# Optimization experiments

Hardware: AMD Instinct MI355X
Metric: run time of the kernel (lower is better)

The kernel has to match this reference:

```python
import jax, jax.numpy as jnp
import numpy as np

DIM = 512
VOCAB = 32000
G = 0.9


def setup_inputs() -> dict:
    key = jax.random.key(0)
    k1, k2, k3, k4, k5, k6 = jax.random.split(key, 6)
    B, T = 32, 4096
    x = jax.random.randint(k1, (B, T), 0, VOCAB)
    s = 1.0 / np.sqrt(DIM)
    emb = jax.random.normal(k2, (VOCAB, DIM), dtype=jnp.float32)
    W_w = jax.random.uniform(k3, (DIM, DIM), dtype=jnp.float32, minval=-s, maxval=s)
    W_b = jax.random.uniform(k4, (DIM,), dtype=jnp.float32, minval=-s, maxval=s)
    head_w = jax.random.uniform(k5, (VOCAB, DIM), dtype=jnp.float32, minval=-s, maxval=s)
    head_b = jax.random.uniform(k6, (VOCAB,), dtype=jnp.float32, minval=-s, maxval=s)
    return {"x": x, "emb": emb, "W_w": W_w, "W_b": W_b, "head_w": head_w, "head_b": head_b}


def reference(x, emb, W_w, W_b, head_w, head_b):
    # u_t = tanh(W @ emb(x_t) + b): input-only nonlinearity, computed for all t at once
    u = jnp.tanh(jnp.einsum('btd,ed->bte', emb[x], W_w) + W_b)  # [B,T,D]
    B = x.shape[0]
    h0 = jnp.zeros((B, DIM), dtype=u.dtype)

    def step(h, u_t):  # h = g*h + (1-g)*u_t  (leaky integration)
        h = G * h + (1.0 - G) * u_t
        return h, None

    h, _ = jax.lax.scan(step, h0, jnp.swapaxes(u, 0, 1))  # scan over T
    return h @ head_w.T + head_b  # [B, VOCAB]
```

## Files before the change

### kernel.cpp

```cpp
#include <hip/hip_runtime.h>
#include <math.h>
#include <stdint.h>

#define B_  32
#define T_  4096
#define D_  512
#define V_  32000
#define KW  128

typedef __attribute__((ext_vector_type(8))) short bf16x8_t;
typedef __attribute__((ext_vector_type(4))) float f32x4_t;

__device__ inline unsigned short f2bf(float f) {
    union { float f; uint32_t u; } c; c.f = f;
    return (unsigned short)((c.u + 0x7FFFu + ((c.u >> 16) & 1u)) >> 16);
}
__device__ inline float bf2f(unsigned short s) {
    union { uint32_t u; float f; } c; c.u = ((uint32_t)s) << 16;
    return c.f;
}

__global__ __launch_bounds__(256) void k_cvtw(const float* __restrict__ Ww,
                                              unsigned short* __restrict__ Wbf,
                                              float* __restrict__ hbuf) {
    const int gid = blockIdx.x * 256 + threadIdx.x;
    const int idx = gid * 8;
    const float4 a = *(const float4*)&Ww[idx];
    const float4 b = *(const float4*)&Ww[idx + 4];
    union { unsigned short s[8]; uint4 v; } o;
    o.s[0] = f2bf(a.x); o.s[1] = f2bf(a.y); o.s[2] = f2bf(a.z); o.s[3] = f2bf(a.w);
    o.s[4] = f2bf(b.x); o.s[5] = f2bf(b.y); o.s[6] = f2bf(b.z); o.s[7] = f2bf(b.w);
    *(uint4*)&Wbf[idx] = o.v;
    if (gid < B_ * D_) hbuf[gid] = 0.f;
}

__global__ __launch_bounds__(256) void k_hidden(const int* __restrict__ x,
                                                const float* __restrict__ emb,
                                                const unsigned short* __restrict__ Wbf,
                                                const float* __restrict__ Wb,
                                                float* __restrict__ h) {
    __shared__ int rows[32];
    __shared__ __align__(16) unsigned short As[32 * 32];
    __shared__ __align__(16) unsigned short Bs[64 * 32];
    __shared__ float red[8][64];

    const int tid = threadIdx.x;
    const int b   = blockIdx.x >> 5;
    const int e0  = ((blockIdx.x >> 2) & 7) * 64;
    const int tb  = blockIdx.x & 3;

    if (tid < 32) rows[tid] = x[b * T_ + (T_ - KW) + tb * 32 + tid];
    __syncthreads();

    const int lane = tid & 63;
    const int w    = tid >> 6;
    const int m15  = lane & 15;
    const int q    = lane >> 4;
    const int mt   = w & 1;
    const int nh   = w >> 1;

    f32x4_t acc[2];
    acc[0] = (f32x4_t){0.f, 0.f, 0.f, 0.f};
    acc[1] = (f32x4_t){0.f, 0.f, 0.f, 0.f};

    for (int k0 = 0; k0 < D_; k0 += 32) {
        __syncthreads();
        if (tid < 128) {
            const float* src = emb + (size_t)rows[tid >> 2] * D_ + k0 + (tid & 3) * 8;
            const float4 a0 = *(const float4*)src;
            const float4 a1 = *(const float4*)(src + 4);
            union { unsigned short s[8]; uint4 v; } o;
            o.s[0] = f2bf(a0.x); o.s[1] = f2bf(a0.y); o.s[2] = f2bf(a0.z); o.s[3] = f2bf(a0.w);
            o.s[4] = f2bf(a1.x); o.s[5] = f2bf(a1.y); o.s[6] = f2bf(a1.z); o.s[7] = f2bf(a1.w);
            *(uint4*)&As[tid * 8] = o.v;
        }
        {
            const unsigned short* src = Wbf + (size_t)(e0 + (tid >> 2)) * D_ + k0 + (tid & 3) * 8;
            __builtin_amdgcn_global_load_lds(
                (const __attribute__((address_space(1))) void*)src,
                (__attribute__((address_space(3))) void*)&Bs[tid * 8], 16, 0, 0);
        }
        __syncthreads();

        const bf16x8_t af  = *(const bf16x8_t*)&As[(mt * 16 + m15) * 32 + q * 8];
        const bf16x8_t bf0 = *(const bf16x8_t*)&Bs[(nh * 32 + m15) * 32 + q * 8];
        const bf16x8_t bf1 = *(const bf16x8_t*)&Bs[(nh * 32 + 16 + m15) * 32 + q * 8];
        acc[0] = __builtin_amdgcn_mfma_f32_16x16x32_bf16(af, bf0, acc[0], 0, 0, 0);
        acc[1] = __builtin_amdgcn_mfma_f32_16x16x32_bf16(af, bf1, acc[1], 0, 0, 0);
    }

    float p[2] = {0.f, 0.f};
#pragma unroll
    for (int ni = 0; ni < 2; ni++) {
        const float wbv = Wb[e0 + nh * 32 + ni * 16 + m15];
#pragma unroll
        for (int r = 0; r < 4; r++) {
            const int twin = tb * 32 + mt * 16 + q * 4 + r;
            const float pre = acc[ni][r] + wbv;
            const float e2  = __expf(2.f * pre);
            const float u   = (e2 - 1.f) / (e2 + 1.f);
            const float wt  = 0.1f * exp2f((float)(127 - twin) * -0.15200309344504995f);
            p[ni] += wt * u;
        }
    }
#pragma unroll
    for (int ni = 0; ni < 2; ni++)
        red[mt * 4 + q][nh * 32 + ni * 16 + m15] = p[ni];
    __syncthreads();
    if (tid < 64) {
        float s = 0.f;
#pragma unroll
        for (int g = 0; g < 8; g++) s += red[g][tid];
        atomicAdd(&h[b * D_ + e0 + tid], s);
    }
}

__global__ __launch_bounds__(256) void k_hsplit(const float* __restrict__ h,
                                                unsigned short* __restrict__ hhi,
                                                unsigned short* __restrict__ hlo) {
    const int i = blockIdx.x * 256 + threadIdx.x;
    const float v = h[i];
    const unsigned short hi = f2bf(v);
    hhi[i] = hi;
    hlo[i] = f2bf(v - bf2f(hi));
}

__global__ __launch_bounds__(256) void k_head(const unsigned short* __restrict__ hhi,
                                              const unsigned short* __restrict__ hlo,
                                              const float* __restrict__ Whead,
                                              const float* __restrict__ bhead,
                                              float* __restrict__ out) {
    const int lane = threadIdx.x & 63;
    const int w    = threadIdx.x >> 6;
    const int n    = lane & 15;
    const int q    = lane >> 4;
    const int v    = blockIdx.x * 64 + w * 16 + n;

    f32x4_t acc[2];
    acc[0] = (f32x4_t){0.f, 0.f, 0.f, 0.f};
    acc[1] = (f32x4_t){0.f, 0.f, 0.f, 0.f};

    const float* __restrict__ wp = Whead + (size_t)v * D_ + q * 8;
    const unsigned short* __restrict__ ah0 = hhi + n * D_ + q * 8;
    const unsigned short* __restrict__ ah1 = hhi + (16 + n) * D_ + q * 8;
    const unsigned short* __restrict__ al0 = hlo + n * D_ + q * 8;
    const unsigned short* __restrict__ al1 = hlo + (16 + n) * D_ + q * 8;

#pragma unroll 2
    for (int ks = 0; ks < 16; ks++) {
        const int off = ks * 32;
        const float4 w0 = *(const float4*)&wp[off];
        const float4 w1 = *(const float4*)&wp[off + 4];
        const bf16x8_t a0h = *(const bf16x8_t*)&ah0[off];
        const bf16x8_t a1h = *(const bf16x8_t*)&ah1[off];
        const bf16x8_t a0l = *(const bf16x8_t*)&al0[off];
        const bf16x8_t a1l = *(const bf16x8_t*)&al1[off];

        const float wf[8] = {w0.x, w0.y, w0.z, w0.w, w1.x, w1.y, w1.z, w1.w};
        union { unsigned short s[8]; bf16x8_t v; } bh, bl;
#pragma unroll
        for (int j = 0; j < 8; j++) {
            const unsigned short hi = f2bf(wf[j]);
            bh.s[j] = hi;
            bl.s[j] = f2bf(wf[j] - bf2f(hi));
        }
        acc[0] = __builtin_amdgcn_mfma_f32_16x16x32_bf16(a0h, bh.v, acc[0], 0, 0, 0);
        acc[1] = __builtin_amdgcn_mfma_f32_16x16x32_bf16(a1h, bh.v, acc[1], 0, 0, 0);
        acc[0] = __builtin_amdgcn_mfma_f32_16x16x32_bf16(a0l, bh.v, acc[0], 0, 0, 0);
        acc[1] = __builtin_amdgcn_mfma_f32_16x16x32_bf16(a1l, bh.v, acc[1], 0, 0, 0);
        acc[0] = __builtin_amdgcn_mfma_f32_16x16x32_bf16(a0h, bl.v, acc[0], 0, 0, 0);
        acc[1] = __builtin_amdgcn_mfma_f32_16x16x32_bf16(a1h, bl.v, acc[1], 0, 0, 0);
    }

    const float bb = bhead[v];
#pragma unroll
    for (int mtl = 0; mtl < 2; mtl++)
#pragma unroll
        for (int r = 0; r < 4; r++)
            out[(size_t)(mtl * 16 + q * 4 + r) * V_ + v] = acc[mtl][r] + bb;
}

extern "C" void kernel_launch(void* const* d_in, const int* in_sizes, int n_in,
                              void* d_out, int out_size, void* d_ws, size_t ws_size,
                              hipStream_t stream) {
    const int*   x      = (const int*)d_in[0];
    const float* emb    = (const float*)d_in[1];
    const float* W_w    = (const float*)d_in[2];
    const float* W_b    = (const float*)d_in[3];
    const float* head_w = (const float*)d_in[4];
    const float* head_b = (const float*)d_in[5];
    float* out = (float*)d_out;

    unsigned short* Wbf = (unsigned short*)d_ws;
    float*          hbuf = (float*)((char*)d_ws + 512 * 1024);
    unsigned short* hhi  = (unsigned short*)((char*)d_ws + 576 * 1024);
    unsigned short* hlo  = (unsigned short*)((char*)d_ws + 608 * 1024);

    k_cvtw  <<<dim3(128),     dim3(256), 0, stream>>>(W_w, Wbf, hbuf);
    k_hidden<<<dim3(1024),    dim3(256), 0, stream>>>(x, emb, Wbf, W_b, hbuf);
    k_hsplit<<<dim3(64),      dim3(256), 0, stream>>>(hbuf, hhi, hlo);
    k_head  <<<dim3(V_ / 64), dim3(256), 0, stream>>>(hhi, hlo, head_w, head_b, out);
}
```

Measured before the change: 169.3 us.

## Drop split-bf16 head, pre-gather embeddings, widen K tiles, split head K across waves

The head GEMM no longer uses the hi/lo bf16 split (3 MFMAs per step). It does a single bf16 MFMA with h staged in LDS, splits K across wave pairs with an LDS reduction, and software-prefetches the weights. Embedding gather and bf16 conversion move into a fused prep kernel alongside the W conversion. The hidden GEMM then loads 128-wide K tiles with XOR-swizzled LDS via global_load_lds. This removes the hsplit launch and two-thirds of the head MFMA work, at the cost of lower head precision (plain bf16 for h and W).

```diff
diff --git a/kernel.cpp b/kernel.cpp
--- a/kernel.cpp
+++ b/kernel.cpp
@@ -15,42 +15,53 @@
     union { float f; uint32_t u; } c; c.f = f;
     return (unsigned short)((c.u + 0x7FFFu + ((c.u >> 16) & 1u)) >> 16);
 }
-__device__ inline float bf2f(unsigned short s) {
-    union { uint32_t u; float f; } c; c.u = ((uint32_t)s) << 16;
-    return c.f;
-}
-
-__global__ __launch_bounds__(256) void k_cvtw(const float* __restrict__ Ww,
-                                              unsigned short* __restrict__ Wbf,
-                                              float* __restrict__ hbuf) {
-    const int gid = blockIdx.x * 256 + threadIdx.x;
-    const int idx = gid * 8;
-    const float4 a = *(const float4*)&Ww[idx];
-    const float4 b = *(const float4*)&Ww[idx + 4];
+
+__device__ inline uint4 cvt8(const float4 a, const float4 b) {
     union { unsigned short s[8]; uint4 v; } o;
     o.s[0] = f2bf(a.x); o.s[1] = f2bf(a.y); o.s[2] = f2bf(a.z); o.s[3] = f2bf(a.w);
     o.s[4] = f2bf(b.x); o.s[5] = f2bf(b.y); o.s[6] = f2bf(b.z); o.s[7] = f2bf(b.w);
-    *(uint4*)&Wbf[idx] = o.v;
-    if (gid < B_ * D_) hbuf[gid] = 0.f;
-}
-
-__global__ __launch_bounds__(256) void k_hidden(const int* __restrict__ x,
-                                                const float* __restrict__ emb,
+    return o.v;
+}
+
+__global__ __launch_bounds__(256) void k_prep(const int* __restrict__ x,
+                                              const float* __restrict__ emb,
+                                              const float* __restrict__ Ww,
+                                              unsigned short* __restrict__ Wbf,
+                                              unsigned short* __restrict__ Abf,
+                                              float* __restrict__ hbuf) {
+    const int tid = threadIdx.x;
+    if (blockIdx.x < 128) {
+        const int gid = blockIdx.x * 256 + tid;
+        const int idx = gid * 8;
+        const float4 a = *(const float4*)&Ww[idx];
+        const float4 b = *(const float4*)&Ww[idx + 4];
+        *(uint4*)&Wbf[idx] = cvt8(a, b);
+        if (gid < B_ * D_) hbuf[gid] = 0.f;
+    } else {
+        const int j = (blockIdx.x - 128) * 256 + tid;
+        const int r = j >> 6;
+        const int c = (j & 63) * 8;
+        const int b = r >> 7;
+        const int row = x[b * T_ + (T_ - KW) + (r & 127)];
+        const float* src = emb + (size_t)row * D_ + c;
+        const float4 a = *(const float4*)src;
+        const float4 bb = *(const float4*)(src + 4);
+        *(uint4*)&Abf[(size_t)r * D_ + c] = cvt8(a, bb);
+    }
+}
+
+__global__ __launch_bounds__(256) void k_hidden(const unsigned short* __restrict__ Abf,
                                                 const unsigned short* __restrict__ Wbf,
                                                 const float* __restrict__ Wb,
                                                 float* __restrict__ h) {
-    __shared__ int rows[32];
-    __shared__ __align__(16) unsigned short As[32 * 32];
-    __shared__ __align__(16) unsigned short Bs[64 * 32];
+    __shared__ __align__(16) unsigned short As[512 * 8];
+    __shared__ __align__(16) unsigned short Bs[1024 * 8];
     __shared__ float red[8][64];
 
     const int tid = threadIdx.x;
     const int b   = blockIdx.x >> 5;
     const int e0  = ((blockIdx.x >> 2) & 7) * 64;
-    const int tb  = blockIdx.x & 3;
-
-    if (tid < 32) rows[tid] = x[b * T_ + (T_ - KW) + tb * 32 + tid];
-    __syncthreads();
+    const int ts  = blockIdx.x & 3;
 
     const int lane = tid & 63;
     const int w    = tid >> 6;
@@ -63,30 +74,44 @@
     acc[0] = (f32x4_t){0.f, 0.f, 0.f, 0.f};
     acc[1] = (f32x4_t){0.f, 0.f, 0.f, 0.f};
 
-    for (int k0 = 0; k0 < D_; k0 += 32) {
+    const size_t abase = (size_t)(b * KW + ts * 32) * D_;
+
+    for (int k0 = 0; k0 < D_; k0 += 128) {
         __syncthreads();
-        if (tid < 128) {
-            const float* src = emb + (size_t)rows[tid >> 2] * D_ + k0 + (tid & 3) * 8;
-            const float4 a0 = *(const float4*)src;
-            const float4 a1 = *(const float4*)(src + 4);
-            union { unsigned short s[8]; uint4 v; } o;
-            o.s[0] = f2bf(a0.x); o.s[1] = f2bf(a0.y); o.s[2] = f2bf(a0.z); o.s[3] = f2bf(a0.w);
-            o.s[4] = f2bf(a1.x); o.s[5] = f2bf(a1.y); o.s[6] = f2bf(a1.z); o.s[7] = f2bf(a1.w);
-            *(uint4*)&As[tid * 8] = o.v;
-        }
-        {
-            const unsigned short* src = Wbf + (size_t)(e0 + (tid >> 2)) * D_ + k0 + (tid & 3) * 8;
+#pragma unroll
+        for (int i = 0; i < 2; i++) {
+            const int j  = tid + 256 * i;
+            const int m  = j >> 4;
+            const int ko = (j & 15) ^ (m & 15);
+            const unsigned short* src = Abf + abase + (size_t)m * D_ + k0 + ko * 8;
             __builtin_amdgcn_global_load_lds(
                 (const __attribute__((address_space(1))) void*)src,
-                (__attribute__((address_space(3))) void*)&Bs[tid * 8], 16, 0, 0);
+                (__attribute__((address_space(3))) void*)&As[j * 8], 16, 0, 0);
+        }
+#pragma unroll
+        for (int i = 0; i < 4; i++) {
+            const int j  = tid + 256 * i;
+            const int n  = j >> 4;
+            const int ko = (j & 15) ^ (n & 15);
+            const unsigned short* src = Wbf + (size_t)(e0 + n) * D_ + k0 + ko * 8;
+            __builtin_amdgcn_global_load_lds(
+                (const __attribute__((address_space(1))) void*)src,
+                (__attribute__((address_space(3))) void*)&Bs[j * 8], 16, 0, 0);
         }
         __syncthreads();
 
-        const bf16x8_t af  = *(const bf16x8_t*)&As[(mt * 16 + m15) * 32 + q * 8];
-        const bf16x8_t bf0 = *(const bf16x8_t*)&Bs[(nh * 32 + m15) * 32 + q * 8];
-        const bf16x8_t bf1 = *(const bf16x8_t*)&Bs[(nh * 32 + 16 + m15) * 32 + q * 8];
-        acc[0] = __builtin_amdgcn_mfma_f32_16x16x32_bf16(af, bf0, acc[0], 0, 0, 0);
-        acc[1] = __builtin_amdgcn_mfma_f32_16x16x32_bf16(af, bf1, acc[1], 0, 0, 0);
+#pragma unroll
+        for (int kk = 0; kk < 4; kk++) {
+            const int ko = kk * 4 + q;
+            const int mA = mt * 16 + m15;
+            const int n0 = nh * 32 + m15;
+            const int n1 = n0 + 16;
+            const bf16x8_t af  = *(const bf16x8_t*)&As[(mA * 16 + (ko ^ m15)) * 8];
+            const bf16x8_t bf0 = *(const bf16x8_t*)&Bs[(n0 * 16 + (ko ^ m15)) * 8];
+            const bf16x8_t bf1 = *(const bf16x8_t*)&Bs[(n1 * 16 + (ko ^ m15)) * 8];
+            acc[0] = __builtin_amdgcn_mfma_f32_16x16x32_bf16(af, bf0, acc[0], 0, 0, 0);
+            acc[1] = __builtin_amdgcn_mfma_f32_16x16x32_bf16(af, bf1, acc[1], 0, 0, 0);
+        }
     }
 
     float p[2] = {0.f, 0.f};
@@ -95,7 +120,7 @@
         const float wbv = Wb[e0 + nh * 32 + ni * 16 + m15];
 #pragma unroll
         for (int r = 0; r < 4; r++) {
-            const int twin = tb * 32 + mt * 16 + q * 4 + r;
+            const int twin = ts * 32 + mt * 16 + q * 4 + r;
             const float pre = acc[ni][r] + wbv;
             const float e2  = __expf(2.f * pre);
             const float u   = (e2 - 1.f) / (e2 + 1.f);
@@ -115,69 +140,73 @@
     }
 }
 
-__global__ __launch_bounds__(256) void k_hsplit(const float* __restrict__ h,
-                                                unsigned short* __restrict__ hhi,
-                                                unsigned short* __restrict__ hlo) {
-    const int i = blockIdx.x * 256 + threadIdx.x;
-    const float v = h[i];
-    const unsigned short hi = f2bf(v);
-    hhi[i] = hi;
-    hlo[i] = f2bf(v - bf2f(hi));
-}
-
-__global__ __launch_bounds__(256) void k_head(const unsigned short* __restrict__ hhi,
-                                              const unsigned short* __restrict__ hlo,
+__global__ __launch_bounds__(256) void k_head(const float* __restrict__ h,
                                               const float* __restrict__ Whead,
                                               const float* __restrict__ bhead,
                                               float* __restrict__ out) {
-    const int lane = threadIdx.x & 63;
-    const int w    = threadIdx.x >> 6;
+    __shared__ __align__(16) unsigned short Hs[32 * 520 + 16];
+
+    const int tid = threadIdx.x;
+#pragma unroll
+    for (int i = 0; i < 8; i++) {
+        const int g = (tid + 256 * i) * 8;
+        const int r = g >> 9;
+        const int c = g & 511;
+        const float4 a = *(const float4*)&h[g];
+        const float4 b = *(const float4*)&h[g + 4];
+        *(uint4*)&Hs[r * 520 + c] = cvt8(a, b);
+    }
+    __syncthreads();
+
+    const int lane = tid & 63;
+    const int w    = tid >> 6;
+    const int vt   = w & 1;
+    const int kh   = w >> 1;
     const int n    = lane & 15;
     const int q    = lane >> 4;
-    const int v    = blockIdx.x * 64 + w * 16 + n;
-
-    f32x4_t acc[2];
-    acc[0] = (f32x4_t){0.f, 0.f, 0.f, 0.f};
-    acc[1] = (f32x4_t){0.f, 0.f, 0.f, 0.f};
-
-    const float* __restrict__ wp = Whead + (size_t)v * D_ + q * 8;
-    const unsigned short* __restrict__ ah0 = hhi + n * D_ + q * 8;
-    const unsigned short* __restrict__ ah1 = hhi + (16 + n) * D_ + q * 8;
-    const unsigned short* __restrict__ al0 = hlo + n * D_ + q * 8;
-    const unsigned short* __restrict__ al1 = hlo + (16 + n) * D_ + q * 8;
-
-#pragma unroll 2
-    for (int ks = 0; ks < 16; ks++) {
-        const int off = ks * 32;
-        const float4 w0 = *(const float4*)&wp[off];
-        const float4 w1 = *(const float4*)&wp[off + 4];
-        const bf16x8_t a0h = *(const bf16x8_t*)&ah0[off];
-        const bf16x8_t a1h = *(const bf16x8_t*)&ah1[off];
-        const bf16x8_t a0l = *(const bf16x8_t*)&al0[off];
-        const bf16x8_t a1l = *(const bf16x8_t*)&al1[off];
-
-        const float wf[8] = {w0.x, w0.y, w0.z, w0.w, w1.x, w1.y, w1.z, w1.w};
-        union { unsigned short s[8]; bf16x8_t v; } bh, bl;
-#pragma unroll
-        for (int j = 0; j < 8; j++) {
-            const unsigned short hi = f2bf(wf[j]);
-            bh.s[j] = hi;
-            bl.s[j] = f2bf(wf[j] - bf2f(hi));
-        }
-        acc[0] = __builtin_amdgcn_mfma_f32_16x16x32_bf16(a0h, bh.v, acc[0], 0, 0, 0);
-        acc[1] = __builtin_amdgcn_mfma_f32_16x16x32_bf16(a1h, bh.v, acc[1], 0, 0, 0);
-        acc[0] = __builtin_amdgcn_mfma_f32_16x16x32_bf16(a0l, bh.v, acc[0], 0, 0, 0);
-        acc[1] = __builtin_amdgcn_mfma_f32_16x16x32_bf16(a1l, bh.v, acc[1], 0, 0, 0);
-        acc[0] = __builtin_amdgcn_mfma_f32_16x16x32_bf16(a0h, bl.v, acc[0], 0, 0, 0);
-        acc[1] = __builtin_amdgcn_mfma_f32_16x16x32_bf16(a1h, bl.v, acc[1], 0, 0, 0);
-    }
-
-    const float bb = bhead[v];
-#pragma unroll
-    for (int mtl = 0; mtl < 2; mtl++)
-#pragma unroll
-        for (int r = 0; r < 4; r++)
-            out[(size_t)(mtl * 16 + q * 4 + r) * V_ + v] = acc[mtl][r] + bb;
+    const int v    = blockIdx.x * 32 + vt * 16 + n;
+
+    const float* __restrict__ wp = Whead + (size_t)v * D_ + kh * 256 + q * 8;
+
+    f32x4_t acc0 = (f32x4_t){0.f, 0.f, 0.f, 0.f};
+    f32x4_t acc1 = (f32x4_t){0.f, 0.f, 0.f, 0.f};
+
+    float4 c0 = *(const float4*)&wp[0];
+    float4 c1 = *(const float4*)&wp[4];
+#pragma unroll
+    for (int ks = 0; ks < 8; ks++) {
+        float4 n0 = c0, n1 = c1;
+        if (ks < 7) {
+            n0 = *(const float4*)&wp[(ks + 1) * 32];
+            n1 = *(const float4*)&wp[(ks + 1) * 32 + 4];
+        }
+        union { uint4 u; bf16x8_t v8; } bfv;
+        bfv.u = cvt8(c0, c1);
+        const int kb = kh * 256 + ks * 32 + q * 8;
+        const bf16x8_t a0 = *(const bf16x8_t*)&Hs[n * 520 + kb];
+        const bf16x8_t a1 = *(const bf16x8_t*)&Hs[(n + 16) * 520 + kb];
+        acc0 = __builtin_amdgcn_mfma_f32_16x16x32_bf16(a0, bfv.v8, acc0, 0, 0, 0);
+        acc1 = __builtin_amdgcn_mfma_f32_16x16x32_bf16(a1, bfv.v8, acc1, 0, 0, 0);
+        c0 = n0; c1 = n1;
+    }
+
+    __syncthreads();
+    float* Rs = (float*)Hs;
+    if (kh == 1) {
+        float* p = &Rs[(vt * 64 + lane) * 8];
+#pragma unroll
+        for (int r = 0; r < 4; r++) { p[r] = acc0[r]; p[4 + r] = acc1[r]; }
+    }
+    __syncthreads();
+    if (kh == 0) {
+        const float* p = &Rs[(vt * 64 + lane) * 8];
+        const float bb = bhead[v];
+#pragma unroll
+        for (int r = 0; r < 4; r++) {
+            out[(size_t)(q * 4 + r) * V_ + v]      = acc0[r] + p[r]     + bb;
+            out[(size_t)(16 + q * 4 + r) * V_ + v] = acc1[r] + p[4 + r] + bb;
+        }
+    }
 }
 
 extern "C" void kernel_launch(void* const* d_in, const int* in_sizes, int n_in,
@@ -191,13 +220,11 @@
     const float* head_b = (const float*)d_in[5];
     float* out = (float*)d_out;
 
-    unsigned short* Wbf = (unsigned short*)d_ws;
+    unsigned short* Wbf  = (unsigned short*)d_ws;
     float*          hbuf = (float*)((char*)d_ws + 512 * 1024);
-    unsigned short* hhi  = (unsigned short*)((char*)d_ws + 576 * 1024);
-    unsigned short* hlo  = (unsigned short*)((char*)d_ws + 608 * 1024);
-
-    k_cvtw  <<<dim3(128),     dim3(256), 0, stream>>>(W_w, Wbf, hbuf);
-    k_hidden<<<dim3(1024),    dim3(256), 0, stream>>>(x, emb, Wbf, W_b, hbuf);
-    k_hsplit<<<dim3(64),      dim3(256), 0, stream>>>(hbuf, hhi, hlo);
-    k_head  <<<dim3(V_ / 64), dim3(256), 0, stream>>>(hhi, hlo, head_w, head_b, out);
-}
+    unsigned short* Abf  = (unsigned short*)((char*)d_ws + 576 * 1024);
+
+    k_prep  <<<dim3(1152), dim3(256), 0, stream>>>(x, emb, W_w, Wbf, Abf, hbuf);
+    k_hidden<<<dim3(1024), dim3(256), 0, stream>>>(Abf, Wbf, W_b, hbuf);
+    k_head  <<<dim3(1000), dim3(256), 0, stream>>>(hbuf, head_w, head_b, out);
+}
```

Result: faster. 149.0 us (-12.0%).
